# Kernel tuning notes

Hardware: AMD Instinct MI355X
Metric: run time of the kernel (lower is better)

## Reference

```python
import jax, jax.numpy as jnp
import numpy as np

NUM_EXPERTS = 8
HIDDEN = 1024
FFN = 2048
TOKENS = 2048


def setup_inputs() -> dict:
    key = jax.random.key(0)
    k_x, k_idx, k_w1, k_w2 = jax.random.split(key, 4)
    scale = 0.02
    x = jax.random.normal(k_x, (TOKENS, HIDDEN), dtype=jnp.float32)
    expert_indices = jax.random.randint(k_idx, (TOKENS,), 0, NUM_EXPERTS, dtype=jnp.int64)
    W1 = jax.random.normal(k_w1, (NUM_EXPERTS, HIDDEN, FFN), dtype=jnp.float32) * scale
    b1 = jnp.zeros((NUM_EXPERTS, FFN), dtype=jnp.float32)
    W2 = jax.random.normal(k_w2, (NUM_EXPERTS, FFN, HIDDEN), dtype=jnp.float32) * scale
    b2 = jnp.zeros((NUM_EXPERTS, HIDDEN), dtype=jnp.float32)
    return {"x": x, "expert_indices": expert_indices, "W1": W1, "b1": b1, "W2": W2, "b2": b2}


def reference(x, expert_indices, W1, b1, W2, b2):
    # Each token routed to one expert's MLP: Linear -> GELU(exact) -> Linear.
    # Dropout is identity in eval mode. Loop is over the small fixed expert set.
    out = jnp.zeros_like(x)
    for e in range(NUM_EXPERTS):
        h = jax.nn.gelu(x @ W1[e] + b1[e], approximate=False)  # [T, FFN]
        y = h @ W2[e] + b2[e]                                   # [T, H]
        mask = (expert_indices == e)[:, None]
        out = out + jnp.where(mask, y, 0.0)
    return out
```

## Files before the change

### kernel.cpp

```cpp
#include <hip/hip_runtime.h>

#define T_TOK 2048
#define HID   1024
#define FFN   2048
#define NEXP  8

typedef __attribute__((ext_vector_type(8))) short bf16x8;
typedef __attribute__((ext_vector_type(4))) float f32x4;

__device__ __forceinline__ short f2bf(float f) {
    unsigned u = __builtin_bit_cast(unsigned, f);
    u = (u + 0x7fffu + ((u >> 16) & 1u)) >> 16;
    return (short)u;
}

__device__ __forceinline__ float gelu_exact(float x) {
    return 0.5f * x * (1.0f + erff(x * 0.70710678118654752f));
}

__device__ __forceinline__ int swz(int row, int k) {
    return row * 64 + ((((k >> 3) + row) & 7) << 3) + (k & 7);
}

__global__ void bucket_kernel(const int* __restrict__ idx,
                              int* __restrict__ offs, int* __restrict__ cnts,
                              int* __restrict__ tokl) {
    __shared__ int c[NEXP], cur[NEXP], o[NEXP];
    int tid = threadIdx.x;
    if (tid < NEXP) { c[tid] = 0; cur[tid] = 0; }
    __syncthreads();
    for (int t = tid; t < T_TOK; t += 256) atomicAdd(&c[idx[t]], 1);
    __syncthreads();
    if (tid == 0) {
        int s = 0;
        for (int e = 0; e < NEXP; e++) { o[e] = s; s += c[e]; }
    }
    __syncthreads();
    if (tid < NEXP) { offs[tid] = o[tid]; cnts[tid] = c[tid]; }
    for (int t = tid; t < T_TOK; t += 256) {
        int e = idx[t];
        int p = o[e] + atomicAdd(&cur[e], 1);
        tokl[p] = t;
    }
}

__global__ __launch_bounds__(256) void xcvt_kernel(const float* __restrict__ x,
                                                   short* __restrict__ xb) {
    int i = (blockIdx.x * 256 + threadIdx.x) * 8;
    float4 v0 = *(const float4*)(x + i);
    float4 v1 = *(const float4*)(x + i + 4);
    bf16x8 r = {f2bf(v0.x), f2bf(v0.y), f2bf(v0.z), f2bf(v0.w),
                f2bf(v1.x), f2bf(v1.y), f2bf(v1.z), f2bf(v1.w)};
    *(bf16x8*)(xb + i) = r;
}

__global__ __launch_bounds__(256) void initout_kernel(const int* __restrict__ idx,
                                                      const float* __restrict__ b2,
                                                      float* __restrict__ out) {
    int t = blockIdx.x;
    int e = idx[t];
    const float4* src = (const float4*)(b2 + (size_t)e * HID);
    float4* dst = (float4*)(out + (size_t)t * HID);
    dst[threadIdx.x] = src[threadIdx.x];
}

__global__ __launch_bounds__(256) void gemm1_kernel(
        const short* __restrict__ xb, const float* __restrict__ W1,
        const float* __restrict__ b1,
        const int* __restrict__ offs, const int* __restrict__ cnts,
        const int* __restrict__ tokl, short* __restrict__ hg) {
    int e = blockIdx.z;
    int count = cnts[e];
    int t0 = blockIdx.y * 64;
    if (t0 >= count) return;
    int off = offs[e];
    int n0 = blockIdx.x * 64;

    __shared__ short As[2][64 * 64];
    __shared__ short Bs[2][64 * 64];
    __shared__ int stok[64];

    int tid = threadIdx.x;
    if (tid < 64) {
        int p = t0 + tid;
        stok[tid] = tokl[off + (p < count ? p : count - 1)];
    }
    __syncthreads();

    const float* Bsrc = W1 + (size_t)e * HID * FFN + n0;

    int w = tid >> 6, lane = tid & 63, l15 = lane & 15, quad = lane >> 4;
    int wm = (w >> 1) * 32, wn = (w & 1) * 32;
    int ar = tid >> 3, ac = (tid & 7) * 8;
    int bn = tid & 63, bw = tid >> 6;

    f32x4 acc[2][2];
#pragma unroll
    for (int i = 0; i < 2; i++)
#pragma unroll
        for (int j = 0; j < 2; j++) acc[i][j] = (f32x4){0.f, 0.f, 0.f, 0.f};

    bf16x8 pA0, pA1;
    float pB[16];

#define G1_LOADA(K0) { \
    pA0 = *(const bf16x8*)(xb + (size_t)stok[ar] * HID + (K0) + ac); \
    pA1 = *(const bf16x8*)(xb + (size_t)stok[ar + 32] * HID + (K0) + ac); }
#define G1_LOADB(K0) { \
    _Pragma("unroll") for (int i = 0; i < 4; i++) \
    _Pragma("unroll") for (int j = 0; j < 4; j++) \
        pB[i * 4 + j] = Bsrc[(size_t)((K0) + bw * 16 + i * 4 + j) * FFN + bn]; }
#define G1_STORE(BUF) { \
    *(bf16x8*)&As[BUF][swz(ar, ac)] = pA0; \
    *(bf16x8*)&As[BUF][swz(ar + 32, ac)] = pA1; \
    _Pragma("unroll") for (int i = 0; i < 4; i++) { \
        short4 s = make_short4(f2bf(pB[i*4]), f2bf(pB[i*4+1]), f2bf(pB[i*4+2]), f2bf(pB[i*4+3])); \
        *(short4*)&Bs[BUF][swz(bn, bw * 16 + i * 4)] = s; } }

    G1_LOADA(0); G1_LOADB(0);
    G1_STORE(0);
    __syncthreads();

    for (int kt = 0; kt < 16; kt++) {
        int cur = kt & 1;
        if (kt < 15) { G1_LOADA((kt + 1) * 64); G1_LOADB((kt + 1) * 64); }
#pragma unroll
        for (int kk = 0; kk < 2; kk++) {
            int kc = kk * 32 + quad * 8;
            bf16x8 a0 = *(const bf16x8*)&As[cur][swz(wm + l15, kc)];
            bf16x8 a1 = *(const bf16x8*)&As[cur][swz(wm + 16 + l15, kc)];
            bf16x8 b0 = *(const bf16x8*)&Bs[cur][swz(wn + l15, kc)];
            bf16x8 b1v = *(const bf16x8*)&Bs[cur][swz(wn + 16 + l15, kc)];
            acc[0][0] = __builtin_amdgcn_mfma_f32_16x16x32_bf16(a0, b0, acc[0][0], 0, 0, 0);
            acc[0][1] = __builtin_amdgcn_mfma_f32_16x16x32_bf16(a0, b1v, acc[0][1], 0, 0, 0);
            acc[1][0] = __builtin_amdgcn_mfma_f32_16x16x32_bf16(a1, b0, acc[1][0], 0, 0, 0);
            acc[1][1] = __builtin_amdgcn_mfma_f32_16x16x32_bf16(a1, b1v, acc[1][1], 0, 0, 0);
        }
        __syncthreads();
        if (kt < 15) G1_STORE(1 - cur);
        __syncthreads();
    }

#pragma unroll
    for (int mt = 0; mt < 2; mt++) {
        int rbase = wm + mt * 16 + quad * 4;
#pragma unroll
        for (int nt = 0; nt < 2; nt++) {
            int coln = n0 + wn + nt * 16 + l15;
            float bb = b1[e * FFN + coln];
#pragma unroll
            for (int r = 0; r < 4; r++) {
                int p = t0 + rbase + r;
                if (p < count) {
                    float hv = gelu_exact(acc[mt][nt][r] + bb);
                    hg[(size_t)(off + p) * FFN + coln] = f2bf(hv);
                }
            }
        }
    }
}

__global__ __launch_bounds__(256) void gemm2_kernel(
        const short* __restrict__ hg, const float* __restrict__ W2,
        const int* __restrict__ offs, const int* __restrict__ cnts,
        const int* __restrict__ tokl, float* __restrict__ out) {
    int e = blockIdx.z & 7;
    int ks = blockIdx.z >> 3;
    int count = cnts[e];
    int t0 = blockIdx.y * 64;
    if (t0 >= count) return;
    int off = offs[e];
    int n0 = blockIdx.x * 64;
    int kbase = ks * (FFN / 2);

    __shared__ short As[2][64 * 64];
    __shared__ short Bs[2][64 * 64];

    int tid = threadIdx.x;
    const float* Bsrc = W2 + (size_t)e * FFN * HID + n0;

    int w = tid >> 6, lane = tid & 63, l15 = lane & 15, quad = lane >> 4;
    int wm = (w >> 1) * 32, wn = (w & 1) * 32;
    int ar = tid >> 3, ac = (tid & 7) * 8;
    int bn = tid & 63, bw = tid >> 6;

    int ga0 = off + (t0 + ar      < count ? t0 + ar      : count - 1);
    int ga1 = off + (t0 + ar + 32 < count ? t0 + ar + 32 : count - 1);

    f32x4 acc[2][2];
#pragma unroll
    for (int i = 0; i < 2; i++)
#pragma unroll
        for (int j = 0; j < 2; j++) acc[i][j] = (f32x4){0.f, 0.f, 0.f, 0.f};

    bf16x8 pA0, pA1;
    float pB[16];

#define G2_LOADA(K0) { \
    pA0 = *(const bf16x8*)(hg + (size_t)ga0 * FFN + (K0) + ac); \
    pA1 = *(const bf16x8*)(hg + (size_t)ga1 * FFN + (K0) + ac); }
#define G2_LOADB(K0) { \
    _Pragma("unroll") for (int i = 0; i < 4; i++) \
    _Pragma("unroll") for (int j = 0; j < 4; j++) \
        pB[i * 4 + j] = Bsrc[(size_t)((K0) + bw * 16 + i * 4 + j) * HID + bn]; }
#define G2_STORE(BUF) { \
    *(bf16x8*)&As[BUF][swz(ar, ac)] = pA0; \
    *(bf16x8*)&As[BUF][swz(ar + 32, ac)] = pA1; \
    _Pragma("unroll") for (int i = 0; i < 4; i++) { \
        short4 s = make_short4(f2bf(pB[i*4]), f2bf(pB[i*4+1]), f2bf(pB[i*4+2]), f2bf(pB[i*4+3])); \
        *(short4*)&Bs[BUF][swz(bn, bw * 16 + i * 4)] = s; } }

    G2_LOADA(kbase); G2_LOADB(kbase);
    G2_STORE(0);
    __syncthreads();

    for (int kt = 0; kt < 16; kt++) {
        int cur = kt & 1;
        if (kt < 15) { G2_LOADA(kbase + (kt + 1) * 64); G2_LOADB(kbase + (kt + 1) * 64); }
#pragma unroll
        for (int kk = 0; kk < 2; kk++) {
            int kc = kk * 32 + quad * 8;
            bf16x8 a0 = *(const bf16x8*)&As[cur][swz(wm + l15, kc)];
            bf16x8 a1 = *(const bf16x8*)&As[cur][swz(wm + 16 + l15, kc)];
            bf16x8 b0 = *(const bf16x8*)&Bs[cur][swz(wn + l15, kc)];
            bf16x8 b1v = *(const bf16x8*)&Bs[cur][swz(wn + 16 + l15, kc)];
            acc[0][0] = __builtin_amdgcn_mfma_f32_16x16x32_bf16(a0, b0, acc[0][0], 0, 0, 0);
            acc[0][1] = __builtin_amdgcn_mfma_f32_16x16x32_bf16(a0, b1v, acc[0][1], 0, 0, 0);
            acc[1][0] = __builtin_amdgcn_mfma_f32_16x16x32_bf16(a1, b0, acc[1][0], 0, 0, 0);
            acc[1][1] = __builtin_amdgcn_mfma_f32_16x16x32_bf16(a1, b1v, acc[1][1], 0, 0, 0);
        }
        __syncthreads();
        if (kt < 15) G2_STORE(1 - cur);
        __syncthreads();
    }

#pragma unroll
    for (int mt = 0; mt < 2; mt++) {
        int rbase = wm + mt * 16 + quad * 4;
#pragma unroll
        for (int nt = 0; nt < 2; nt++) {
            int coln = n0 + wn + nt * 16 + l15;
#pragma unroll
            for (int r = 0; r < 4; r++) {
                int p = t0 + rbase + r;
                if (p < count) {
                    int tok = tokl[off + p];
                    atomicAdd(out + (size_t)tok * HID + coln, acc[mt][nt][r]);
                }
            }
        }
    }
}

extern "C" void kernel_launch(void* const* d_in, const int* in_sizes, int n_in,
                              void* d_out, int out_size, void* d_ws, size_t ws_size,
                              hipStream_t stream) {
    const float* x   = (const float*)d_in[0];
    const int*   idx = (const int*)d_in[1];
    const float* W1  = (const float*)d_in[2];
    const float* b1  = (const float*)d_in[3];
    const float* W2  = (const float*)d_in[4];
    const float* b2  = (const float*)d_in[5];
    float* out = (float*)d_out;

    const size_t META = 32768;
    int*   offs = (int*)d_ws;
    int*   cnts = offs + 8;
    int*   tokl = offs + 16;
    short* xb   = (short*)((char*)d_ws + META);
    short* hg   = (short*)((char*)d_ws + META + (size_t)T_TOK * HID * 2);

    bucket_kernel<<<1, 256, 0, stream>>>(idx, offs, cnts, tokl);
    xcvt_kernel<<<T_TOK * HID / (256 * 8), 256, 0, stream>>>(x, xb);
    initout_kernel<<<T_TOK, 256, 0, stream>>>(idx, b2, out);

    gemm1_kernel<<<dim3(FFN / 64, T_TOK / 64, NEXP), 256, 0, stream>>>(
        xb, W1, b1, offs, cnts, tokl, hg);
    gemm2_kernel<<<dim3(HID / 64, T_TOK / 64, NEXP * 2), 256, 0, stream>>>(
        hg, W2, offs, cnts, tokl, out);
}
```

Measured before the change: 247.9 us.

## Compact expert tile grid via slot table and drop one barrier per k-step

The bucket kernel now writes a compact list of (expert, token-tile) slots, and both GEMMs launch over at most 40 slots instead of 8x32 mostly-empty tiles. This removes the launch and scheduling cost of many early-exit blocks. The main loops also go from two __syncthreads per k-iteration to one, relying on the double buffer to keep reads of the current stage separate from writes to the next. MAX_SLOTS=40 assumes per-expert counts fit (sum of ceil(count/64) ≤ 40). That holds for roughly uniform routing but would silently drop tiles for skewed routing.

```diff
diff --git a/kernel.cpp b/kernel.cpp
--- a/kernel.cpp
+++ b/kernel.cpp
@@ -4,6 +4,7 @@
 #define HID   1024
 #define FFN   2048
 #define NEXP  8
+#define MAX_SLOTS 40
 
 typedef __attribute__((ext_vector_type(8))) short bf16x8;
 typedef __attribute__((ext_vector_type(4))) float f32x4;
@@ -24,7 +25,8 @@
 
 __global__ void bucket_kernel(const int* __restrict__ idx,
                               int* __restrict__ offs, int* __restrict__ cnts,
-                              int* __restrict__ tokl) {
+                              int* __restrict__ tokl,
+                              int* __restrict__ slot_e, int* __restrict__ slot_t0) {
     __shared__ int c[NEXP], cur[NEXP], o[NEXP];
     int tid = threadIdx.x;
     if (tid < NEXP) { c[tid] = 0; cur[tid] = 0; }
@@ -34,6 +36,12 @@
     if (tid == 0) {
         int s = 0;
         for (int e = 0; e < NEXP; e++) { o[e] = s; s += c[e]; }
+        int ns = 0;
+        for (int e = 0; e < NEXP; e++)
+            for (int t0 = 0; t0 < c[e]; t0 += 64) {
+                slot_e[ns] = e; slot_t0[ns] = t0; ns++;
+            }
+        for (; ns < MAX_SLOTS; ns++) slot_e[ns] = -1;
     }
     __syncthreads();
     if (tid < NEXP) { offs[tid] = o[tid]; cnts[tid] = c[tid]; }
@@ -68,11 +76,14 @@
         const short* __restrict__ xb, const float* __restrict__ W1,
         const float* __restrict__ b1,
         const int* __restrict__ offs, const int* __restrict__ cnts,
-        const int* __restrict__ tokl, short* __restrict__ hg) {
-    int e = blockIdx.z;
+        const int* __restrict__ tokl,
+        const int* __restrict__ slot_e, const int* __restrict__ slot_t0,
+        short* __restrict__ hg) {
+    int s = blockIdx.y;
+    int e = slot_e[s];
+    if (e < 0) return;
+    int t0 = slot_t0[s];
     int count = cnts[e];
-    int t0 = blockIdx.y * 64;
-    if (t0 >= count) return;
     int off = offs[e];
     int n0 = blockIdx.x * 64;
 
@@ -114,14 +125,14 @@
     *(bf16x8*)&As[BUF][swz(ar, ac)] = pA0; \
     *(bf16x8*)&As[BUF][swz(ar + 32, ac)] = pA1; \
     _Pragma("unroll") for (int i = 0; i < 4; i++) { \
-        short4 s = make_short4(f2bf(pB[i*4]), f2bf(pB[i*4+1]), f2bf(pB[i*4+2]), f2bf(pB[i*4+3])); \
-        *(short4*)&Bs[BUF][swz(bn, bw * 16 + i * 4)] = s; } }
+        short4 sv = make_short4(f2bf(pB[i*4]), f2bf(pB[i*4+1]), f2bf(pB[i*4+2]), f2bf(pB[i*4+3])); \
+        *(short4*)&Bs[BUF][swz(bn, bw * 16 + i * 4)] = sv; } }
 
     G1_LOADA(0); G1_LOADB(0);
     G1_STORE(0);
-    __syncthreads();
 
     for (int kt = 0; kt < 16; kt++) {
+        __syncthreads();
         int cur = kt & 1;
         if (kt < 15) { G1_LOADA((kt + 1) * 64); G1_LOADB((kt + 1) * 64); }
 #pragma unroll
@@ -136,9 +147,7 @@
             acc[1][0] = __builtin_amdgcn_mfma_f32_16x16x32_bf16(a1, b0, acc[1][0], 0, 0, 0);
             acc[1][1] = __builtin_amdgcn_mfma_f32_16x16x32_bf16(a1, b1v, acc[1][1], 0, 0, 0);
         }
-        __syncthreads();
         if (kt < 15) G1_STORE(1 - cur);
-        __syncthreads();
     }
 
 #pragma unroll
@@ -163,12 +172,15 @@
 __global__ __launch_bounds__(256) void gemm2_kernel(
         const short* __restrict__ hg, const float* __restrict__ W2,
         const int* __restrict__ offs, const int* __restrict__ cnts,
-        const int* __restrict__ tokl, float* __restrict__ out) {
-    int e = blockIdx.z & 7;
-    int ks = blockIdx.z >> 3;
+        const int* __restrict__ tokl,
+        const int* __restrict__ slot_e, const int* __restrict__ slot_t0,
+        float* __restrict__ out) {
+    int s = blockIdx.y;
+    int e = slot_e[s];
+    if (e < 0) return;
+    int t0 = slot_t0[s];
+    int ks = blockIdx.z;
     int count = cnts[e];
-    int t0 = blockIdx.y * 64;
-    if (t0 >= count) return;
     int off = offs[e];
     int n0 = blockIdx.x * 64;
     int kbase = ks * (FFN / 2);
@@ -207,14 +219,14 @@
     *(bf16x8*)&As[BUF][swz(ar, ac)] = pA0; \
     *(bf16x8*)&As[BUF][swz(ar + 32, ac)] = pA1; \
     _Pragma("unroll") for (int i = 0; i < 4; i++) { \
-        short4 s = make_short4(f2bf(pB[i*4]), f2bf(pB[i*4+1]), f2bf(pB[i*4+2]), f2bf(pB[i*4+3])); \
-        *(short4*)&Bs[BUF][swz(bn, bw * 16 + i * 4)] = s; } }
+        short4 sv = make_short4(f2bf(pB[i*4]), f2bf(pB[i*4+1]), f2bf(pB[i*4+2]), f2bf(pB[i*4+3])); \
+        *(short4*)&Bs[BUF][swz(bn, bw * 16 + i * 4)] = sv; } }
 
     G2_LOADA(kbase); G2_LOADB(kbase);
     G2_STORE(0);
-    __syncthreads();
 
     for (int kt = 0; kt < 16; kt++) {
+        __syncthreads();
         int cur = kt & 1;
         if (kt < 15) { G2_LOADA(kbase + (kt + 1) * 64); G2_LOADB(kbase + (kt + 1) * 64); }
 #pragma unroll
@@ -229,9 +241,7 @@
             acc[1][0] = __builtin_amdgcn_mfma_f32_16x16x32_bf16(a1, b0, acc[1][0], 0, 0, 0);
             acc[1][1] = __builtin_amdgcn_mfma_f32_16x16x32_bf16(a1, b1v, acc[1][1], 0, 0, 0);
         }
-        __syncthreads();
         if (kt < 15) G2_STORE(1 - cur);
-        __syncthreads();
     }
 
 #pragma unroll
@@ -264,18 +274,20 @@
     float* out = (float*)d_out;
 
     const size_t META = 32768;
-    int*   offs = (int*)d_ws;
-    int*   cnts = offs + 8;
-    int*   tokl = offs + 16;
-    short* xb   = (short*)((char*)d_ws + META);
-    short* hg   = (short*)((char*)d_ws + META + (size_t)T_TOK * HID * 2);
-
-    bucket_kernel<<<1, 256, 0, stream>>>(idx, offs, cnts, tokl);
+    int*   offs    = (int*)d_ws;
+    int*   cnts    = offs + 8;
+    int*   tokl    = offs + 16;
+    int*   slot_e  = offs + 16 + T_TOK;
+    int*   slot_t0 = slot_e + MAX_SLOTS;
+    short* xb      = (short*)((char*)d_ws + META);
+    short* hg      = (short*)((char*)d_ws + META + (size_t)T_TOK * HID * 2);
+
+    bucket_kernel<<<1, 256, 0, stream>>>(idx, offs, cnts, tokl, slot_e, slot_t0);
     xcvt_kernel<<<T_TOK * HID / (256 * 8), 256, 0, stream>>>(x, xb);
     initout_kernel<<<T_TOK, 256, 0, stream>>>(idx, b2, out);
 
-    gemm1_kernel<<<dim3(FFN / 64, T_TOK / 64, NEXP), 256, 0, stream>>>(
-        xb, W1, b1, offs, cnts, tokl, hg);
-    gemm2_kernel<<<dim3(HID / 64, T_TOK / 64, NEXP * 2), 256, 0, stream>>>(
-        hg, W2, offs, cnts, tokl, out);
-}
+    gemm1_kernel<<<dim3(FFN / 64, MAX_SLOTS), 256, 0, stream>>>(
+        xb, W1, b1, offs, cnts, tokl, slot_e, slot_t0, hg);
+    gemm2_kernel<<<dim3(HID / 64, MAX_SLOTS, 2), 256, 0, stream>>>(
+        hg, W2, offs, cnts, tokl, slot_e, slot_t0, out);
+}
```

After: 245.2 us. About the same (-1.1%).
